# Optimization experiments

Hardware: AMD Instinct MI355X
Metric: run time of the kernel (lower is better)

## Reference

```python
import jax, jax.numpy as jnp
import numpy as np

# dims (see shape_source): seq S = d_t+1 must equal d_k for the unary quantum loader
B, T, D_IN = 128, 127, 48
DK = 128
S = T + 1            # tokens incl. class token; S == DK
H, L = 8, 6
P = (S * S - S) // 2  # RBS angles per head (pyramid circuit over S wires)


def _pyramid_pairs(n):
    # deterministic pyramid ordering of n(n-1)/2 adjacent-pair Givens rotations
    a, b = [], []
    for k in range(n - 1):
        for i in range(k, -1, -1):
            a.append(i)
            b.append(i + 1)
    return np.asarray(a, np.int32), np.asarray(b, np.int32)


def _build_W(phi, pa, pb, n):
    # classical simulation of the RBS pyramid circuit restricted to the unary
    # subspace: product of Givens rotations -> orthogonal n x n matrix
    def step(W, inp):
        ia, ib, th = inp
        c, s = jnp.cos(th), jnp.sin(th)
        ra, rb = W[ia], W[ib]
        W = W.at[ia].set(c * ra - s * rb)
        W = W.at[ib].set(s * ra + c * rb)
        return W, None
    W0 = jnp.eye(n, dtype=phi.dtype)
    W, _ = jax.lax.scan(step, W0, (pa, pb, phi))
    return W


def _layer_norm(x, g, b, eps=1e-5):
    m = jnp.mean(x, axis=-1, keepdims=True)
    v = jnp.mean((x - m) ** 2, axis=-1, keepdims=True)
    return (x - m) * jax.lax.rsqrt(v + eps) * g + b


def setup_inputs() -> dict:
    key = jax.random.key(0)
    ks = jax.random.split(key, 8)
    f32 = jnp.float32
    return {
        "x": jax.random.normal(ks[0], (B, T, D_IN), f32),
        "embed_w": jax.random.normal(ks[1], (DK, D_IN), f32) / np.sqrt(D_IN),
        "embed_b": jnp.zeros((DK,), f32),
        "class_token": jax.random.normal(ks[2], (DK,), f32) / DK,
        "norm0_g": jnp.ones((DK,), f32),
        "norm0_b": jnp.zeros((DK,), f32),
        "Vw": jax.random.normal(ks[3], (L, H, DK, DK), f32) / np.sqrt(DK),
        "Vb": jnp.zeros((L, H, DK), f32),
        "ln_g": jnp.ones((L, H, DK), f32),
        "ln_b": jnp.zeros((L, H, DK), f32),
        "phi": jax.random.normal(ks[4], (L, H, P), f32) / np.sqrt(S),
        "merger_w": jax.random.normal(ks[5], (L, H), f32) / np.sqrt(H),
        "merger_b": jnp.zeros((L,), f32),
    }


def reference(x, embed_w, embed_b, class_token, norm0_g, norm0_b,
              Vw, Vb, ln_g, ln_b, phi, merger_w, merger_b):
    Bsz = x.shape[0]
    pa, pb = _pyramid_pairs(S)
    # orthogonal score matrices for every (layer, head)
    Ws = jax.vmap(lambda p: _build_W(p, pa, pb, S))(phi.reshape(L * H, P))
    Ws = Ws.reshape(L, H, S, S)

    # embed patches, prepend class token (pos_embedding add is a no-op in the
    # original source: bare `+self.pos_embedding` statement, so it is omitted)
    tok = jnp.einsum('btf,df->btd', x, embed_w) + embed_b
    h = jnp.concatenate([jnp.broadcast_to(class_token, (Bsz, 1, DK)), tok], axis=1)
    h = _layer_norm(h, norm0_g, norm0_b)

    scale = 1.0 / np.sqrt(DK)
    for l in range(L):
        nrm = jnp.sqrt(jnp.sum(h * h, axis=-1))      # input3: token norms [B,S]
        u = h / nrm[..., None]                        # unit tokens (convert_array)
        hh, nn, uu = h, nrm, u

        def head(W, vw, vb, g, be):
            V = jnp.einsum('bsd,ed->bse', hh, vw) + vb
            M = jnp.einsum('bsd,de,bte->bst', uu, W, uu)
            A = (M * M) * (nn[:, :, None] * nn[:, None, :])
            Pm = jax.nn.softmax(A * scale, axis=-1)
            return _layer_norm(jnp.einsum('bst,btd->bsd', Pm, V) + hh, g, be)

        hs = jax.vmap(head)(Ws[l], Vw[l], Vb[l], ln_g[l], ln_b[l])  # [H,B,S,D]
        h = jnp.einsum('hbsd,h->bsd', hs, merger_w[l]) + merger_b[l]
    return h[:, -1, :]
```

## Files before the change

### kernel.cpp

```cpp
#include <hip/hip_runtime.h>
#include <hip/hip_bf16.h>


typedef __bf16 bf16x8 __attribute__((ext_vector_type(8)));
typedef float  f32x4  __attribute__((ext_vector_type(4)));
typedef unsigned int u32;

__device__ __forceinline__ int sidx(int row, int col)
{
    return row * 128 + ((((col >> 3) ^ (row & 15)) << 3) | (col & 7));
}

__global__ void __launch_bounds__(256)
prep_kernel(const float* __restrict__ phi, float2* __restrict__ csn,
            const float* __restrict__ vw,  __bf16* __restrict__ cvwf)
{
    if (blockIdx.x < 3072) {
        const int mat = blockIdx.x >> 6;
        const int t   = ((blockIdx.x & 63) << 2) + (threadIdx.x >> 6);
        const int j   = threadIdx.x & 63;
        float th = 0.f;
        if (t < 253) {
            const int p = t & 1, i = 2 * j + p;
            const int lim = min(t, 252 - t);
            if (i <= lim) {
                const int k = (t + i) >> 1;
                th = phi[mat * 8128 + ((k * (k + 1)) >> 1) + (k - i)];
            }
        }
        float sn, cs;
        __sincosf(th, &sn, &cs);
        csn[(mat * 256 + t) * 64 + j] = make_float2(cs, sn);
    } else {
        const int f    = (blockIdx.x - 3072) * 256 + threadIdx.x;
        const int lane = f & 63;
        const int k0   = (f >> 6) & 3;
        const int t    = (f >> 8) & 7;
        const int lh   = f >> 11;
        const int row  = t * 16 + (lane & 15);
        const int col  = k0 * 32 + (lane >> 4) * 8;
        const float* src = vw + (lh * 128 + row) * 128 + col;
        __bf16* dst = cvwf + f * 8;
#pragma unroll
        for (int j2 = 0; j2 < 8; j2++) dst[j2] = (__bf16)src[j2];
    }
}

__global__ void __launch_bounds__(64)
build_w_kernel(const float2* __restrict__ csn, __bf16* __restrict__ wt)
{
    const int mat = blockIdx.x >> 5;
    const int grp = blockIdx.x & 31;
    const int c0  = grp * 4;
    const int lam = threadIdx.x;

    const float2* base = csn + (mat * 256) * 64 + lam;

    float vlo[4], vhi[4];
#pragma unroll
    for (int j = 0; j < 4; j++) {
        vlo[j] = (2 * lam     == c0 + j) ? 1.f : 0.f;
        vhi[j] = (2 * lam + 1 == c0 + j) ? 1.f : 0.f;
    }

    float2 buf[3][16];
#pragma unroll
    for (int k = 0; k < 16; k++) buf[0][k] = base[k * 64];
#pragma unroll
    for (int k = 0; k < 16; k++) buf[1][k] = base[(16 + k) * 64];

#pragma unroll
    for (int g = 0; g < 16; g++) {
        const int cb = g % 3;
        if (g < 14) {
            const int nb = (g + 2) % 3;
#pragma unroll
            for (int k = 0; k < 16; k++)
                buf[nb][k] = base[((g + 2) * 16 + k) * 64];
        }
#pragma unroll
        for (int p = 0; p < 8; p++) {
            {
                const float cs = buf[cb][2 * p].x, sn = buf[cb][2 * p].y;
#pragma unroll
                for (int j = 0; j < 4; j++) {
                    float lo = vlo[j], hi = vhi[j];
                    vlo[j] = cs * lo - sn * hi;
                    vhi[j] = sn * lo + cs * hi;
                }
            }
            {
                const float cs = buf[cb][2 * p + 1].x, sn = buf[cb][2 * p + 1].y;
#pragma unroll
                for (int j = 0; j < 4; j++) {
                    float y  = __shfl_down(vlo[j], 1);
                    float x  = vhi[j];
                    float xn = cs * x - sn * y;
                    float yn = sn * x + cs * y;
                    vhi[j] = xn;
                    float z = __shfl_up(yn, 1);
                    if (lam > 0) vlo[j] = z;
                }
            }
        }
    }

    u32* wtu = (u32*)wt;
#pragma unroll
    for (int j = 0; j < 4; j++) {
        __bf16 va = (__bf16)vlo[j];
        __bf16 vb = (__bf16)vhi[j];
        u32 pk = (u32)__builtin_bit_cast(unsigned short, va)
               | ((u32)__builtin_bit_cast(unsigned short, vb) << 16);
        wtu[mat * 8192 + (c0 + j) * 64 + lam] = pk;
    }
}

__global__ void __launch_bounds__(512)
embed_kernel(const float* __restrict__ x,  const float* __restrict__ ew,
             const float* __restrict__ eb, const float* __restrict__ ct,
             const float* __restrict__ g0, const float* __restrict__ b0,
             float* __restrict__ hf, __bf16* __restrict__ hb,
             float* __restrict__ invn)
{
    __shared__ float sx[4][48];
    __shared__ float sred[4][2];
    const int d  = threadIdx.x & 127, sq = threadIdx.x >> 7;
    const int wh = (threadIdx.x >> 6) & 1;
    const int b  = blockIdx.x & 127;
    const int s  = (blockIdx.x >> 7) * 4 + sq;

    if (s > 0 && d < 48) sx[sq][d] = x[(b * 127 + (s - 1)) * 48 + d];
    __syncthreads();

    float val;
    if (s == 0) {
        val = ct[d];
    } else {
        float aa = 0.f;
#pragma unroll
        for (int f = 0; f < 48; f++) aa = fmaf(sx[sq][f], ew[d * 48 + f], aa);
        val = aa + eb[d];
    }
    float v = val;
#pragma unroll
    for (int m = 32; m; m >>= 1) v += __shfl_xor(v, m);
    if ((threadIdx.x & 63) == 0) sred[sq][wh] = v;
    __syncthreads();
    float mean = (sred[sq][0] + sred[sq][1]) * (1.f / 128.f);
    float xc   = val - mean;
    __syncthreads();
    v = xc * xc;
#pragma unroll
    for (int m = 32; m; m >>= 1) v += __shfl_xor(v, m);
    if ((threadIdx.x & 63) == 0) sred[sq][wh] = v;
    __syncthreads();
    float var = (sred[sq][0] + sred[sq][1]) * (1.f / 128.f);
    float y   = xc * rsqrtf(var + 1e-5f) * g0[d] + b0[d];
    __syncthreads();
    v = y * y;
#pragma unroll
    for (int m = 32; m; m >>= 1) v += __shfl_xor(v, m);
    if ((threadIdx.x & 63) == 0) sred[sq][wh] = v;
    __syncthreads();
    float ss = sred[sq][0] + sred[sq][1];

    const int o = (b * 128 + s) * 128 + d;
    hf[o] = y;
    hb[o] = (__bf16)y;
    if (d == 0) invn[b * 128 + s] = rsqrtf(ss);
}

__global__ void __launch_bounds__(512, 4)
attn_kernel(int l,
            const float*  __restrict__ hf,  const __bf16* __restrict__ hb,
            const float*  __restrict__ invn, const __bf16* __restrict__ wt,
            const __bf16* __restrict__ vwf, const float* __restrict__ vb,
            const float* __restrict__ lng,  const float* __restrict__ lnb,
            const float* __restrict__ mwp,  __bf16* __restrict__ hs)
{
    __shared__ __align__(16) __bf16 sH[128 * 128];
    __shared__ __align__(16) __bf16 sY[128 * 128];
    __shared__ float sInv[128];
    __shared__ float sVb[128];
    __shared__ float sLg[128];
    __shared__ float sLb[128];

    const int tid  = threadIdx.x;
    const int lane = tid & 63, w = tid >> 6;
    const int l15  = lane & 15, quad = lane >> 4;
    const int b    = blockIdx.x & 127;
    const int hh   = blockIdx.x >> 7;
    const int lh   = l * 8 + hh;

    const __bf16* hbp = hb + b * 16384;
    const __bf16* wtp = wt + lh * 16384;

#pragma unroll
    for (int c = 0; c < 4; c++) {
        int ch  = tid + c * 512;
        int row = ch >> 4, cc = ch & 15;
        bf16x8 hv = *(const bf16x8*)(hbp + ch * 8);
        bf16x8 wv = *(const bf16x8*)(wtp + ch * 8);
        *(bf16x8*)(&sH[sidx(row, cc * 8)]) = hv;
        *(bf16x8*)(&sY[sidx(row, cc * 8)]) = wv;
    }
    if (tid < 128) {
        sInv[tid] = invn[b * 128 + tid];
        sVb[tid]  = vb[lh * 128 + tid];
        sLg[tid]  = lng[lh * 128 + tid];
        sLb[tid]  = lnb[lh * 128 + tid];
    }
    __syncthreads();

    const int r0 = w * 16;
    const int kq = quad * 8;
    const int q4 = quad * 4;
    const f32x4 vzero = {0.f, 0.f, 0.f, 0.f};

    f32x4 acc[8];

    auto mmL = [&](const __bf16* Ab, const __bf16* Bb) {
#pragma unroll
        for (int t = 0; t < 8; t++) acc[t] = vzero;
#pragma unroll
        for (int k0 = 0; k0 < 128; k0 += 32) {
            const int kk = k0 + kq;
            bf16x8 a0 = *(const bf16x8*)(&Ab[sidx(r0 + l15, kk)]);
#pragma unroll
            for (int t = 0; t < 8; t++) {
                bf16x8 bb = *(const bf16x8*)(&Bb[sidx(t * 16 + l15, kk)]);
                acc[t] = __builtin_amdgcn_mfma_f32_16x16x32_bf16(a0, bb, acc[t], 0, 0, 0);
            }
        }
    };

    mmL(sH, sY);
    __syncthreads();
#pragma unroll
    for (int t = 0; t < 8; t++)
#pragma unroll
        for (int r = 0; r < 4; r++)
            sY[sidx(r0 + q4 + r, t * 16 + l15)] = (__bf16)acc[t][r];

    mmL(sY, sH);

    {
        const float scale2 = 0.08838834764831843f * 1.4426950408889634f;
        float invt[8];
#pragma unroll
        for (int t = 0; t < 8; t++) invt[t] = sInv[t * 16 + l15];
        float invs[4];
#pragma unroll
        for (int r = 0; r < 4; r++) invs[r] = sInv[r0 + q4 + r];

        float mx[4] = {-3e38f, -3e38f, -3e38f, -3e38f};
#pragma unroll
        for (int t = 0; t < 8; t++)
#pragma unroll
            for (int r = 0; r < 4; r++) {
                float g = acc[t][r];
                float v = g * g * invs[r] * invt[t] * scale2;
                acc[t][r] = v;
                mx[r] = fmaxf(mx[r], v);
            }
#pragma unroll
        for (int m = 1; m < 16; m <<= 1)
#pragma unroll
            for (int r = 0; r < 4; r++) mx[r] = fmaxf(mx[r], __shfl_xor(mx[r], m));

        float sm[4] = {0.f, 0.f, 0.f, 0.f};
#pragma unroll
        for (int t = 0; t < 8; t++)
#pragma unroll
            for (int r = 0; r < 4; r++) {
                float e = exp2f(acc[t][r] - mx[r]);
                acc[t][r] = e;
                sm[r] += e;
            }
#pragma unroll
        for (int m = 1; m < 16; m <<= 1)
#pragma unroll
            for (int r = 0; r < 4; r++) sm[r] += __shfl_xor(sm[r], m);
#pragma unroll
        for (int r = 0; r < 4; r++) sm[r] = 1.0f / sm[r];
#pragma unroll
        for (int t = 0; t < 8; t++)
#pragma unroll
            for (int r = 0; r < 4; r++)
                sY[sidx(r0 + q4 + r, t * 16 + l15)] = (__bf16)(acc[t][r] * sm[r]);
    }

    float hres[8][4];
    {
        const float* hfp = hf + (b * 128 + r0 + q4) * 128;
#pragma unroll
        for (int t = 0; t < 8; t++)
#pragma unroll
            for (int r = 0; r < 4; r++)
                hres[t][r] = hfp[r * 128 + t * 16 + l15];
    }

    {
        const __bf16* vbase = vwf + (size_t)lh * 16384;
#pragma unroll
        for (int t = 0; t < 8; t++) acc[t] = vzero;
#pragma unroll
        for (int k0c = 0; k0c < 4; k0c++) {
            const int kk = k0c * 32 + kq;
            bf16x8 a0 = *(const bf16x8*)(&sH[sidx(r0 + l15, kk)]);
#pragma unroll
            for (int t = 0; t < 8; t++) {
                bf16x8 bb = *(const bf16x8*)(vbase + ((t * 4 + k0c) * 64 + lane) * 8);
                acc[t] = __builtin_amdgcn_mfma_f32_16x16x32_bf16(a0, bb, acc[t], 0, 0, 0);
            }
        }
    }
    __syncthreads();

    {
        float vbv[8];
#pragma unroll
        for (int t = 0; t < 8; t++) vbv[t] = sVb[t * 16 + l15];
#pragma unroll
        for (int t = 0; t < 8; t++)
#pragma unroll
            for (int r = 0; r < 4; r++)
                sH[sidx(t * 16 + l15, r0 + q4 + r)] = (__bf16)(acc[t][r] + vbv[t]);
    }
    __syncthreads();

    mmL(sY, sH);

    {
        const float mw = mwp[lh];
        float lgv[8], lbv[8];
#pragma unroll
        for (int t = 0; t < 8; t++) {
            lgv[t] = sLg[t * 16 + l15];
            lbv[t] = sLb[t * 16 + l15];
        }
        float sum_[4] = {0.f, 0.f, 0.f, 0.f};
        float sq_[4]  = {0.f, 0.f, 0.f, 0.f};
#pragma unroll
        for (int t = 0; t < 8; t++)
#pragma unroll
            for (int r = 0; r < 4; r++) {
                float xx = acc[t][r] + hres[t][r];
                acc[t][r] = xx;
                sum_[r] += xx;
                sq_[r]  += xx * xx;
            }
#pragma unroll
        for (int m = 1; m < 16; m <<= 1)
#pragma unroll
            for (int r = 0; r < 4; r++) {
                sum_[r] += __shfl_xor(sum_[r], m);
                sq_[r]  += __shfl_xor(sq_[r], m);
            }
        float mean[4], rstd[4];
#pragma unroll
        for (int r = 0; r < 4; r++) {
            mean[r] = sum_[r] * (1.f / 128.f);
            float var = sq_[r] * (1.f / 128.f) - mean[r] * mean[r];
            rstd[r] = rsqrtf(fmaxf(var, 0.f) + 1e-5f);
        }
        __bf16* hsp = hs + ((hh * 128 + b) * 128 + r0 + q4) * 128;
#pragma unroll
        for (int t = 0; t < 8; t++)
#pragma unroll
            for (int r = 0; r < 4; r++) {
                float y = (acc[t][r] - mean[r]) * rstd[r] * lgv[t] + lbv[t];
                hsp[r * 128 + t * 16 + l15] = (__bf16)(y * mw);
            }
    }
}

__global__ void __launch_bounds__(256)
merge_kernel(const __bf16* __restrict__ hs, const float* __restrict__ mbp, int l,
             float* __restrict__ hf, __bf16* __restrict__ hb, float* __restrict__ invn,
             float* __restrict__ out, int last)
{
    const int b  = blockIdx.x & 127;
    const int s  = (blockIdx.x >> 7) * 4 + (threadIdx.x >> 6);
    const int ln = threadIdx.x & 63;
    const int d2 = ln * 2;

    const float mbv = mbp[l];
    float a0 = mbv, a1 = mbv;
#pragma unroll
    for (int h8 = 0; h8 < 8; h8++) {
        const __bf16* p = hs + (((size_t)h8 * 128 + b) * 128 + s) * 128 + d2;
        a0 += (float)p[0];
        a1 += (float)p[1];
    }
    float v = a0 * a0 + a1 * a1;
#pragma unroll
    for (int m = 32; m; m >>= 1) v += __shfl_xor(v, m);

    const size_t o = ((size_t)b * 128 + s) * 128 + d2;
    *(float2*)(hf + o) = make_float2(a0, a1);
    __bf16 p0 = (__bf16)a0, p1 = (__bf16)a1;
    ((u32*)hb)[o >> 1] = (u32)__builtin_bit_cast(unsigned short, p0)
                       | ((u32)__builtin_bit_cast(unsigned short, p1) << 16);
    if (ln == 0) invn[b * 128 + s] = rsqrtf(v);
    if (last && s == 127) *(float2*)(out + b * 128 + d2) = make_float2(a0, a1);
}

extern "C" void kernel_launch(void* const* d_in, const int* in_sizes, int n_in,
                              void* d_out, int out_size, void* d_ws, size_t ws_size,
                              hipStream_t stream)
{
    (void)in_sizes; (void)n_in; (void)out_size; (void)ws_size;

    const float* x   = (const float*)d_in[0];
    const float* ew  = (const float*)d_in[1];
    const float* eb  = (const float*)d_in[2];
    const float* ct  = (const float*)d_in[3];
    const float* g0  = (const float*)d_in[4];
    const float* b0  = (const float*)d_in[5];
    const float* vw  = (const float*)d_in[6];
    const float* vb  = (const float*)d_in[7];
    const float* lng = (const float*)d_in[8];
    const float* lnb = (const float*)d_in[9];
    const float* phi = (const float*)d_in[10];
    const float* mw  = (const float*)d_in[11];
    const float* mb  = (const float*)d_in[12];
    float* out = (float*)d_out;

    char* ws = (char*)d_ws;
    __bf16* wt   = (__bf16*)(ws);
    float*  hf   = (float*)(ws + 1572864);
    __bf16* hb   = (__bf16*)(ws + 9961472);
    float*  invn = (float*)(ws + 14155776);
    __bf16* hs   = (__bf16*)(ws + 14221312);
    __bf16* cvwf = (__bf16*)(ws + 47775744);
    float2* csn  = (float2*)(ws + 49348608);

    prep_kernel<<<3456, 256, 0, stream>>>(phi, csn, vw, cvwf);
    build_w_kernel<<<1536, 64, 0, stream>>>(csn, wt);
    embed_kernel<<<4096, 512, 0, stream>>>(x, ew, eb, ct, g0, b0, hf, hb, invn);
    for (int l = 0; l < 6; l++) {
        attn_kernel<<<1024, 512, 0, stream>>>(l, hf, hb, invn, wt, cvwf, vb,
                                              lng, lnb, mw, hs);
        merge_kernel<<<4096, 256, 0, stream>>>(hs, mb, l, hf, hb, invn, out,
                                               (l == 5) ? 1 : 0);
    }
}
```

Before: 423.5 us.

## Skip unused rows in last layer, stream W from global, async LDS loads

Only the final token row feeds the output, so in the last layer the attention kernel computes scores and outputs only for the wave owning row 127, and the merge kernel runs only 32 blocks that write the output directly. The W matrix is stored in MFMA fragment order and read straight from global memory, like Vw, instead of being staged through LDS. H is now staged with global_load_lds direct-to-LDS copies, and the MFMA loops are wrapped in s_setprio. The result is more divergent code paths, and the pre-swizzled global_load_lds layout must match sidx exactly.

```diff
diff --git a/kernel.cpp b/kernel.cpp
--- a/kernel.cpp
+++ b/kernel.cpp
@@ -9,6 +9,13 @@
 __device__ __forceinline__ int sidx(int row, int col)
 {
     return row * 128 + ((((col >> 3) ^ (row & 15)) << 3) | (col & 7));
+}
+
+__device__ __forceinline__ void gll16(const void* g, void* l)
+{
+    __builtin_amdgcn_global_load_lds(
+        (const __attribute__((address_space(1))) void*)g,
+        (__attribute__((address_space(3))) void*)l, 16, 0, 0);
 }
 
 __global__ void __launch_bounds__(256)
@@ -105,6 +112,9 @@
         }
     }
 
+    const int t    = c0 >> 4;
+    const int k0w  = lam >> 4;
+    const int quad = (lam >> 2) & 3;
     u32* wtu = (u32*)wt;
 #pragma unroll
     for (int j = 0; j < 4; j++) {
@@ -112,7 +122,8 @@
         __bf16 vb = (__bf16)vhi[j];
         u32 pk = (u32)__builtin_bit_cast(unsigned short, va)
                | ((u32)__builtin_bit_cast(unsigned short, vb) << 16);
-        wtu[mat * 8192 + (c0 + j) * 64 + lam] = pk;
+        const int frag = (t * 4 + k0w) * 64 + quad * 16 + ((c0 & 15) + j);
+        wtu[mat * 8192 + frag * 4 + (lam & 3)] = pk;
     }
 }
 
@@ -172,7 +183,7 @@
 }
 
 __global__ void __launch_bounds__(512, 4)
-attn_kernel(int l,
+attn_kernel(int l, int last,
             const float*  __restrict__ hf,  const __bf16* __restrict__ hb,
             const float*  __restrict__ invn, const __bf16* __restrict__ wt,
             const __bf16* __restrict__ vwf, const float* __restrict__ vb,
@@ -193,17 +204,16 @@
     const int hh   = blockIdx.x >> 7;
     const int lh   = l * 8 + hh;
 
-    const __bf16* hbp = hb + b * 16384;
-    const __bf16* wtp = wt + lh * 16384;
+    const __bf16* hbp   = hb  + b * 16384;
+    const __bf16* wbase = wt  + (size_t)lh * 16384;
+    const __bf16* vbase = vwf + (size_t)lh * 16384;
 
 #pragma unroll
     for (int c = 0; c < 4; c++) {
-        int ch  = tid + c * 512;
-        int row = ch >> 4, cc = ch & 15;
-        bf16x8 hv = *(const bf16x8*)(hbp + ch * 8);
-        bf16x8 wv = *(const bf16x8*)(wtp + ch * 8);
-        *(bf16x8*)(&sH[sidx(row, cc * 8)]) = hv;
-        *(bf16x8*)(&sY[sidx(row, cc * 8)]) = wv;
+        const int ch  = tid + c * 512;
+        const int row = ch >> 4, cc = ch & 15;
+        const int sc  = cc ^ (row & 15);
+        gll16(hbp + (row * 16 + sc) * 8, &sH[(c * 512 + w * 64) * 8]);
     }
     if (tid < 128) {
         sInv[tid] = invn[b * 128 + tid];
@@ -217,12 +227,14 @@
     const int kq = quad * 8;
     const int q4 = quad * 4;
     const f32x4 vzero = {0.f, 0.f, 0.f, 0.f};
+    const bool active = !last || (w == 7);
 
     f32x4 acc[8];
 
     auto mmL = [&](const __bf16* Ab, const __bf16* Bb) {
 #pragma unroll
         for (int t = 0; t < 8; t++) acc[t] = vzero;
+        __builtin_amdgcn_s_setprio(1);
 #pragma unroll
         for (int k0 = 0; k0 < 128; k0 += 32) {
             const int kk = k0 + kq;
@@ -233,89 +245,95 @@
                 acc[t] = __builtin_amdgcn_mfma_f32_16x16x32_bf16(a0, bb, acc[t], 0, 0, 0);
             }
         }
+        __builtin_amdgcn_s_setprio(0);
     };
 
-    mmL(sH, sY);
-    __syncthreads();
-#pragma unroll
-    for (int t = 0; t < 8; t++)
-#pragma unroll
-        for (int r = 0; r < 4; r++)
-            sY[sidx(r0 + q4 + r, t * 16 + l15)] = (__bf16)acc[t][r];
-
-    mmL(sY, sH);
-
-    {
-        const float scale2 = 0.08838834764831843f * 1.4426950408889634f;
-        float invt[8];
-#pragma unroll
-        for (int t = 0; t < 8; t++) invt[t] = sInv[t * 16 + l15];
-        float invs[4];
-#pragma unroll
-        for (int r = 0; r < 4; r++) invs[r] = sInv[r0 + q4 + r];
-
-        float mx[4] = {-3e38f, -3e38f, -3e38f, -3e38f};
-#pragma unroll
-        for (int t = 0; t < 8; t++)
-#pragma unroll
-            for (int r = 0; r < 4; r++) {
-                float g = acc[t][r];
-                float v = g * g * invs[r] * invt[t] * scale2;
-                acc[t][r] = v;
-                mx[r] = fmaxf(mx[r], v);
-            }
-#pragma unroll
-        for (int m = 1; m < 16; m <<= 1)
-#pragma unroll
-            for (int r = 0; r < 4; r++) mx[r] = fmaxf(mx[r], __shfl_xor(mx[r], m));
-
-        float sm[4] = {0.f, 0.f, 0.f, 0.f};
-#pragma unroll
-        for (int t = 0; t < 8; t++)
-#pragma unroll
-            for (int r = 0; r < 4; r++) {
-                float e = exp2f(acc[t][r] - mx[r]);
-                acc[t][r] = e;
-                sm[r] += e;
-            }
-#pragma unroll
-        for (int m = 1; m < 16; m <<= 1)
-#pragma unroll
-            for (int r = 0; r < 4; r++) sm[r] += __shfl_xor(sm[r], m);
-#pragma unroll
-        for (int r = 0; r < 4; r++) sm[r] = 1.0f / sm[r];
-#pragma unroll
-        for (int t = 0; t < 8; t++)
-#pragma unroll
-            for (int r = 0; r < 4; r++)
-                sY[sidx(r0 + q4 + r, t * 16 + l15)] = (__bf16)(acc[t][r] * sm[r]);
-    }
-
-    float hres[8][4];
-    {
-        const float* hfp = hf + (b * 128 + r0 + q4) * 128;
-#pragma unroll
-        for (int t = 0; t < 8; t++)
-#pragma unroll
-            for (int r = 0; r < 4; r++)
-                hres[t][r] = hfp[r * 128 + t * 16 + l15];
-    }
-
-    {
-        const __bf16* vbase = vwf + (size_t)lh * 16384;
+    auto mmG = [&](const __bf16* gB) {
 #pragma unroll
         for (int t = 0; t < 8; t++) acc[t] = vzero;
+        __builtin_amdgcn_s_setprio(1);
 #pragma unroll
         for (int k0c = 0; k0c < 4; k0c++) {
             const int kk = k0c * 32 + kq;
             bf16x8 a0 = *(const bf16x8*)(&sH[sidx(r0 + l15, kk)]);
 #pragma unroll
             for (int t = 0; t < 8; t++) {
-                bf16x8 bb = *(const bf16x8*)(vbase + ((t * 4 + k0c) * 64 + lane) * 8);
+                bf16x8 bb = *(const bf16x8*)(gB + ((t * 4 + k0c) * 64 + lane) * 8);
                 acc[t] = __builtin_amdgcn_mfma_f32_16x16x32_bf16(a0, bb, acc[t], 0, 0, 0);
             }
         }
-    }
+        __builtin_amdgcn_s_setprio(0);
+    };
+
+    float hres[8][4];
+
+    if (active) {
+        mmG(wbase);
+#pragma unroll
+        for (int t = 0; t < 8; t++)
+#pragma unroll
+            for (int r = 0; r < 4; r++)
+                sY[sidx(r0 + q4 + r, t * 16 + l15)] = (__bf16)acc[t][r];
+
+        mmL(sY, sH);
+
+        {
+            const float scale2 = 0.08838834764831843f * 1.4426950408889634f;
+            float invt[8];
+#pragma unroll
+            for (int t = 0; t < 8; t++) invt[t] = sInv[t * 16 + l15];
+            float invs[4];
+#pragma unroll
+            for (int r = 0; r < 4; r++) invs[r] = sInv[r0 + q4 + r];
+
+            float mx[4] = {-3e38f, -3e38f, -3e38f, -3e38f};
+#pragma unroll
+            for (int t = 0; t < 8; t++)
+#pragma unroll
+                for (int r = 0; r < 4; r++) {
+                    float g = acc[t][r];
+                    float v = g * g * invs[r] * invt[t] * scale2;
+                    acc[t][r] = v;
+                    mx[r] = fmaxf(mx[r], v);
+                }
+#pragma unroll
+            for (int m = 1; m < 16; m <<= 1)
+#pragma unroll
+                for (int r = 0; r < 4; r++) mx[r] = fmaxf(mx[r], __shfl_xor(mx[r], m));
+
+            float sm[4] = {0.f, 0.f, 0.f, 0.f};
+#pragma unroll
+            for (int t = 0; t < 8; t++)
+#pragma unroll
+                for (int r = 0; r < 4; r++) {
+                    float e = exp2f(acc[t][r] - mx[r]);
+                    acc[t][r] = e;
+                    sm[r] += e;
+                }
+#pragma unroll
+            for (int m = 1; m < 16; m <<= 1)
+#pragma unroll
+                for (int r = 0; r < 4; r++) sm[r] += __shfl_xor(sm[r], m);
+#pragma unroll
+            for (int r = 0; r < 4; r++) sm[r] = 1.0f / sm[r];
+#pragma unroll
+            for (int t = 0; t < 8; t++)
+#pragma unroll
+                for (int r = 0; r < 4; r++)
+                    sY[sidx(r0 + q4 + r, t * 16 + l15)] = (__bf16)(acc[t][r] * sm[r]);
+        }
+
+        {
+            const float* hfp = hf + (b * 128 + r0 + q4) * 128;
+#pragma unroll
+            for (int t = 0; t < 8; t++)
+#pragma unroll
+                for (int r = 0; r < 4; r++)
+                    hres[t][r] = hfp[r * 128 + t * 16 + l15];
+        }
+    }
+
+    mmG(vbase);
     __syncthreads();
 
     {
@@ -330,49 +348,53 @@
     }
     __syncthreads();
 
-    mmL(sY, sH);
-
-    {
-        const float mw = mwp[lh];
-        float lgv[8], lbv[8];
-#pragma unroll
-        for (int t = 0; t < 8; t++) {
-            lgv[t] = sLg[t * 16 + l15];
-            lbv[t] = sLb[t * 16 + l15];
-        }
-        float sum_[4] = {0.f, 0.f, 0.f, 0.f};
-        float sq_[4]  = {0.f, 0.f, 0.f, 0.f};
-#pragma unroll
-        for (int t = 0; t < 8; t++)
+    if (active) {
+        mmL(sY, sH);
+
+        {
+            const float mw = mwp[lh];
+            float lgv[8], lbv[8];
+#pragma unroll
+            for (int t = 0; t < 8; t++) {
+                lgv[t] = sLg[t * 16 + l15];
+                lbv[t] = sLb[t * 16 + l15];
+            }
+            float sum_[4] = {0.f, 0.f, 0.f, 0.f};
+            float sq_[4]  = {0.f, 0.f, 0.f, 0.f};
+#pragma unroll
+            for (int t = 0; t < 8; t++)
+#pragma unroll
+                for (int r = 0; r < 4; r++) {
+                    float xx = acc[t][r] + hres[t][r];
+                    acc[t][r] = xx;
+                    sum_[r] += xx;
+                    sq_[r]  += xx * xx;
+                }
+#pragma unroll
+            for (int m = 1; m < 16; m <<= 1)
+#pragma unroll
+                for (int r = 0; r < 4; r++) {
+                    sum_[r] += __shfl_xor(sum_[r], m);
+                    sq_[r]  += __shfl_xor(sq_[r], m);
+                }
+            float mean[4], rstd[4];
 #pragma unroll
             for (int r = 0; r < 4; r++) {
-                float xx = acc[t][r] + hres[t][r];
-                acc[t][r] = xx;
-                sum_[r] += xx;
-                sq_[r]  += xx * xx;
-            }
-#pragma unroll
-        for (int m = 1; m < 16; m <<= 1)
-#pragma unroll
-            for (int r = 0; r < 4; r++) {
-                sum_[r] += __shfl_xor(sum_[r], m);
-                sq_[r]  += __shfl_xor(sq_[r], m);
-            }
-        float mean[4], rstd[4];
-#pragma unroll
-        for (int r = 0; r < 4; r++) {
-            mean[r] = sum_[r] * (1.f / 128.f);
-            float var = sq_[r] * (1.f / 128.f) - mean[r] * mean[r];
-            rstd[r] = rsqrtf(fmaxf(var, 0.f) + 1e-5f);
-        }
-        __bf16* hsp = hs + ((hh * 128 + b) * 128 + r0 + q4) * 128;
-#pragma unroll
-        for (int t = 0; t < 8; t++)
-#pragma unroll
-            for (int r = 0; r < 4; r++) {
-                float y = (acc[t][r] - mean[r]) * rstd[r] * lgv[t] + lbv[t];
-                hsp[r * 128 + t * 16 + l15] = (__bf16)(y * mw);
-            }
+                mean[r] = sum_[r] * (1.f / 128.f);
+                float var = sq_[r] * (1.f / 128.f) - mean[r] * mean[r];
+                rstd[r] = rsqrtf(fmaxf(var, 0.f) + 1e-5f);
+            }
+            __bf16* hsp = hs + ((hh * 128 + b) * 128 + r0 + q4) * 128;
+#pragma unroll
+            for (int t = 0; t < 8; t++)
+#pragma unroll
+                for (int r = 0; r < 4; r++) {
+                    if (!last || (q4 + r == 15)) {
+                        float y = (acc[t][r] - mean[r]) * rstd[r] * lgv[t] + lbv[t];
+                        hsp[r * 128 + t * 16 + l15] = (__bf16)(y * mw);
+                    }
+                }
+        }
     }
 }
 
@@ -381,12 +403,19 @@
              float* __restrict__ hf, __bf16* __restrict__ hb, float* __restrict__ invn,
              float* __restrict__ out, int last)
 {
-    const int b  = blockIdx.x & 127;
-    const int s  = (blockIdx.x >> 7) * 4 + (threadIdx.x >> 6);
     const int ln = threadIdx.x & 63;
     const int d2 = ln * 2;
-
     const float mbv = mbp[l];
+
+    int b, s;
+    if (last) {
+        b = blockIdx.x * 4 + (threadIdx.x >> 6);
+        s = 127;
+    } else {
+        b = blockIdx.x & 127;
+        s = (blockIdx.x >> 7) * 4 + (threadIdx.x >> 6);
+    }
+
     float a0 = mbv, a1 = mbv;
 #pragma unroll
     for (int h8 = 0; h8 < 8; h8++) {
@@ -394,6 +423,12 @@
         a0 += (float)p[0];
         a1 += (float)p[1];
     }
+
+    if (last) {
+        *(float2*)(out + b * 128 + d2) = make_float2(a0, a1);
+        return;
+    }
+
     float v = a0 * a0 + a1 * a1;
 #pragma unroll
     for (int m = 32; m; m >>= 1) v += __shfl_xor(v, m);
@@ -404,7 +439,6 @@
     ((u32*)hb)[o >> 1] = (u32)__builtin_bit_cast(unsigned short, p0)
                        | ((u32)__builtin_bit_cast(unsigned short, p1) << 16);
     if (ln == 0) invn[b * 128 + s] = rsqrtf(v);
-    if (last && s == 127) *(float2*)(out + b * 128 + d2) = make_float2(a0, a1);
 }
 
 extern "C" void kernel_launch(void* const* d_in, const int* in_sizes, int n_in,
@@ -441,9 +475,10 @@
     build_w_kernel<<<1536, 64, 0, stream>>>(csn, wt);
     embed_kernel<<<4096, 512, 0, stream>>>(x, ew, eb, ct, g0, b0, hf, hb, invn);
     for (int l = 0; l < 6; l++) {
-        attn_kernel<<<1024, 512, 0, stream>>>(l, hf, hb, invn, wt, cvwf, vb,
-                                              lng, lnb, mw, hs);
-        merge_kernel<<<4096, 256, 0, stream>>>(hs, mb, l, hf, hb, invn, out,
-                                               (l == 5) ? 1 : 0);
-    }
-}
+        const int last = (l == 5) ? 1 : 0;
+        attn_kernel<<<1024, 512, 0, stream>>>(l, last, hf, hb, invn, wt, cvwf,
+                                              vb, lng, lnb, mw, hs);
+        merge_kernel<<<last ? 32 : 4096, 256, 0, stream>>>(hs, mb, l, hf, hb,
+                                                           invn, out, last);
+    }
+}
```

After: 388.5 us. 1.09x faster.
